# Kernel optimization log

Measured on AMD Instinct MI355X. Metric: run time of the kernel, lower is better.

The kernel has to match this reference:

```python
import jax, jax.numpy as jnp
import numpy as np

B, N, K, D = 256, 64, 12, 128


def setup_inputs() -> dict:
    key = jax.random.key(0)
    ks = jax.random.split(key, 12)
    s = 1.0 / np.sqrt(D)
    inp = {
        "nodes_hidden": jax.random.normal(ks[0], (B, N, D), jnp.float32),
        "neighbors_hidden": jax.random.normal(ks[1], (B, N, K, D), jnp.float32),
        # binary neighbor-validity mask (float, as in the torch code)
        "mask": (jax.random.uniform(ks[2], (B, N, K)) < 0.7).astype(jnp.float32),
        "Wq": jax.random.uniform(ks[3], (D, D), jnp.float32, -s, s),
        "bq": jax.random.uniform(ks[4], (D,), jnp.float32, -s, s),
        "Wk": jax.random.uniform(ks[5], (D, D), jnp.float32, -s, s),
        "bk": jax.random.uniform(ks[6], (D,), jnp.float32, -s, s),
        "Wv": jax.random.uniform(ks[7], (D, D), jnp.float32, -s, s),
        "bv": jax.random.uniform(ks[8], (D,), jnp.float32, -s, s),
        # W_att: Linear(2D -> 1); split into the query half and key half of its weight
        "wa_q": jax.random.uniform(ks[9], (D,), jnp.float32, -s, s),
        "wa_k": jax.random.uniform(ks[10], (D,), jnp.float32, -s, s),
        "ba": jax.random.uniform(ks[11], (), jnp.float32, -s, s),
    }
    return inp


def reference(nodes_hidden, neighbors_hidden, mask, Wq, bq, Wk, bk, Wv, bv, wa_q, wa_k, ba):
    # prepend the node itself to its neighbor list: [B,N,K+1,D]
    nh = jnp.concatenate([nodes_hidden[:, :, None, :], neighbors_hidden], axis=2)
    # prepend an always-valid slot to the mask: [B,N,K+1]
    m = jnp.concatenate([jnp.ones(mask.shape[:-1] + (1,), mask.dtype), mask], axis=-1)

    q = nodes_hidden @ Wq + bq            # [B,N,D]
    k = nh @ Wk + bk                      # [B,N,K+1,D]
    v = nh @ Wv + bv                      # [B,N,K+1,D]

    # W_att(cat([q,k])) == q.wa_q + k.wa_k + ba  (avoids materializing the 2D concat)
    sim = (q @ wa_q)[:, :, None] + k @ wa_k + ba   # [B,N,K+1]
    sim = jnp.where(sim >= 0, sim, 0.2 * sim)      # LeakyReLU(0.2)
    sim = jnp.exp(sim) * m                         # masked exp (matches torch exactly)
    attn = sim / (jnp.sum(sim, axis=-1, keepdims=True) + 1e-16)
    return jnp.einsum('bnk,bnkd->bnd', attn, v)    # [B,N,D]
```

## Files before the change

### kernel.cpp

```cpp
#include <hip/hip_runtime.h>


#define B_  256
#define N_  64
#define K_  12
#define D_  128
#define BN  (B_ * N_)
#define ROWS 8
#define HB_STRIDE 132

__global__ void prep_kernel(const float* __restrict__ Wq, const float* __restrict__ bq,
                            const float* __restrict__ Wk, const float* __restrict__ bk,
                            const float* __restrict__ wa_q, const float* __restrict__ wa_k,
                            float* __restrict__ ws) {
    int g = blockIdx.x;
    int l = threadIdx.x;
    const float* row;
    const float* wa;
    float* outp;
    if (g < 128)      { row = Wq + g * D_;         wa = wa_q; outp = ws + g; }
    else if (g < 256) { row = Wk + (g - 128) * D_; wa = wa_k; outp = ws + 128 + (g - 128); }
    else if (g == 256){ row = bq;                  wa = wa_q; outp = ws + 256; }
    else              { row = bk;                  wa = wa_k; outp = ws + 257; }

    float2 r = ((const float2*)row)[l];
    float2 w = ((const float2*)wa)[l];
    float p = r.x * w.x + r.y * w.y;
    #pragma unroll
    for (int m = 1; m < 64; m <<= 1) p += __shfl_xor(p, m, 64);
    if (l == 0) *outp = p;
}

__global__ void __launch_bounds__(256, 4)
fused_kernel(const float* __restrict__ nodes, const float* __restrict__ neigh,
             const float* __restrict__ mask, const float* __restrict__ ba_p,
             const float* __restrict__ ws, const float* __restrict__ Wv,
             const float* __restrict__ bv, float* __restrict__ out) {
    __shared__ float hb[ROWS * HB_STRIDE];
    __shared__ float scL[ROWS];

    const int t    = threadIdx.x;
    const int wave = t >> 6;
    const int l    = t & 63;
    const int li   = l & 31;
    const int h    = l >> 5;
    const int j8   = l & 7;

    const float cq  = ws[256];
    const float ckb = ws[257];
    const float ba  = ba_p[0];
    const float cst = cq + ckb + ba;
    const float4 wqe4 = ((const float4*)ws)[li];
    const float4 wke4 = ((const float4*)(ws + 128))[li];

    for (int p = 0; p < 2; ++p) {
        const int lrow = wave * 2 + p;
        const int idx  = blockIdx.x * ROWS + lrow;

        const float4 nv = ((const float4*)(nodes + (size_t)idx * D_))[li];
        const float4* gp4 = (const float4*)(neigh + (size_t)idx * (K_ * D_));
        float4 x[6];
        #pragma unroll
        for (int i = 0; i < 6; ++i) x[i] = gp4[i * 64 + l];
        const float mval = (j8 < 6) ? mask[(size_t)idx * K_ + 2 * j8 + h] : 0.0f;

        float v[8];
        v[7] = nv.x*wqe4.x + nv.y*wqe4.y + nv.z*wqe4.z + nv.w*wqe4.w;
        v[6] = nv.x*wke4.x + nv.y*wke4.y + nv.z*wke4.z + nv.w*wke4.w;
        #pragma unroll
        for (int i = 0; i < 6; ++i)
            v[i] = x[i].x*wke4.x + x[i].y*wke4.y + x[i].z*wke4.z + x[i].w*wke4.w;

        float a0, a1, a2, a3;
        {
            const bool hi = (l & 1);
            float g0 = hi ? v[0] : v[1];
            float g1 = hi ? v[2] : v[3];
            float g2 = hi ? v[4] : v[5];
            float g3 = hi ? v[6] : v[7];
            g0 = __shfl_xor(g0, 1, 64);
            g1 = __shfl_xor(g1, 1, 64);
            g2 = __shfl_xor(g2, 1, 64);
            g3 = __shfl_xor(g3, 1, 64);
            a0 = (hi ? v[1] : v[0]) + g0;
            a1 = (hi ? v[3] : v[2]) + g1;
            a2 = (hi ? v[5] : v[4]) + g2;
            a3 = (hi ? v[7] : v[6]) + g3;
        }
        float b0, b1;
        {
            const bool hi = (l & 2);
            float g0 = hi ? a0 : a1;
            float g1 = hi ? a2 : a3;
            g0 = __shfl_xor(g0, 2, 64);
            g1 = __shfl_xor(g1, 2, 64);
            b0 = (hi ? a1 : a0) + g0;
            b1 = (hi ? a3 : a2) + g1;
        }
        float c;
        {
            const bool hi = (l & 4);
            float g = hi ? b0 : b1;
            g = __shfl_xor(g, 4, 64);
            c = (hi ? b1 : b0) + g;
        }
        c += __shfl_xor(c, 8, 64);
        c += __shfl_xor(c, 16, 64);

        const float pq  = __shfl(c, 7, 8);
        const float pkn = __shfl(c, 6, 8);
        const float base = pq + cst;

        float s0 = base + pkn;
        s0 = (s0 >= 0.0f) ? s0 : 0.2f * s0;
        const float e0 = __expf(s0);

        float sj = base + c;
        sj = (sj >= 0.0f) ? sj : 0.2f * sj;
        const float ej = (j8 < 6) ? __expf(sj) * mval : 0.0f;

        float Sn = ej;
        Sn += __shfl_xor(Sn, 1, 64);
        Sn += __shfl_xor(Sn, 2, 64);
        Sn += __shfl_xor(Sn, 4, 64);
        Sn += __shfl_xor(Sn, 32, 64);
        const float S   = e0 + Sn;
        const float inv = 1.0f / (S + 1e-16f);
        const float aj  = ej * inv;

        const float an = (h == 0) ? e0 * inv : 0.0f;
        float4 acc;
        acc.x = an * nv.x; acc.y = an * nv.y; acc.z = an * nv.z; acc.w = an * nv.w;
        #pragma unroll
        for (int i = 0; i < 6; ++i) {
            const float ai = __shfl(aj, i, 8);
            acc.x += ai * x[i].x;
            acc.y += ai * x[i].y;
            acc.z += ai * x[i].z;
            acc.w += ai * x[i].w;
        }
        acc.x += __shfl_xor(acc.x, 32, 64);
        acc.y += __shfl_xor(acc.y, 32, 64);
        acc.z += __shfl_xor(acc.z, 32, 64);
        acc.w += __shfl_xor(acc.w, 32, 64);

        if (h == 0) {
            *(float4*)(hb + lrow * HB_STRIDE + 4 * li) = acc;
            if (li == 0) scL[lrow] = S * inv;
        }
    }
    __syncthreads();

    const int rg = t >> 5;
    const int cg = t & 31;
    const float4* wv4 = (const float4*)Wv;
    const float* hrow = hb + rg * HB_STRIDE;

    float4 vacc = make_float4(0.0f, 0.0f, 0.0f, 0.0f);
    #pragma unroll 8
    for (int k = 0; k < D_; ++k) {
        const float a  = hrow[k];
        const float4 w = wv4[k * 32 + cg];
        vacc.x += a * w.x;
        vacc.y += a * w.y;
        vacc.z += a * w.z;
        vacc.w += a * w.w;
    }

    const float4 bvv = ((const float4*)bv)[cg];
    const float  s   = scL[rg];
    float4 o;
    o.x = vacc.x + bvv.x * s;
    o.y = vacc.y + bvv.y * s;
    o.z = vacc.z + bvv.z * s;
    o.w = vacc.w + bvv.w * s;
    *(float4*)(out + (size_t)(blockIdx.x * ROWS + rg) * D_ + cg * 4) = o;
}

extern "C" void kernel_launch(void* const* d_in, const int* in_sizes, int n_in,
                              void* d_out, int out_size, void* d_ws, size_t ws_size,
                              hipStream_t stream) {
    const float* nodes = (const float*)d_in[0];
    const float* neigh = (const float*)d_in[1];
    const float* mask  = (const float*)d_in[2];
    const float* Wq    = (const float*)d_in[3];
    const float* bq    = (const float*)d_in[4];
    const float* Wk    = (const float*)d_in[5];
    const float* bk    = (const float*)d_in[6];
    const float* Wv    = (const float*)d_in[7];
    const float* bv    = (const float*)d_in[8];
    const float* wa_q  = (const float*)d_in[9];
    const float* wa_k  = (const float*)d_in[10];
    const float* ba    = (const float*)d_in[11];
    float* out = (float*)d_out;
    float* ws  = (float*)d_ws;

    prep_kernel<<<258, 64, 0, stream>>>(Wq, bq, Wk, bk, wa_q, wa_k, ws);
    fused_kernel<<<BN / ROWS, 256, 0, stream>>>(nodes, neigh, mask, ba, ws, Wv, bv, out);
}
```

Before: 201.0 us.

## Interleave two rows per wave and defer softmax normalization

Each wave now issues the global loads for both of its rows up front and interleaves their reductions and shuffles, so memory latency for the second row overlaps the first. The softmax sum is taken from the same shuffled weights used to accumulate the weighted values, and normalization is applied once at the end, removing a serial shuffle-reduction before accumulation. The occupancy hint in launch bounds is dropped and the Wv matmul loop unroll is raised. Holding twice the loaded data in registers increases register pressure and may reduce occupancy.

```diff
diff --git a/kernel.cpp b/kernel.cpp
--- a/kernel.cpp
+++ b/kernel.cpp
@@ -31,7 +31,7 @@
     if (l == 0) *outp = p;
 }
 
-__global__ void __launch_bounds__(256, 4)
+__global__ void __launch_bounds__(256)
 fused_kernel(const float* __restrict__ nodes, const float* __restrict__ neigh,
              const float* __restrict__ mask, const float* __restrict__ ba_p,
              const float* __restrict__ ws, const float* __restrict__ Wv,
@@ -53,99 +53,141 @@
     const float4 wqe4 = ((const float4*)ws)[li];
     const float4 wke4 = ((const float4*)(ws + 128))[li];
 
-    for (int p = 0; p < 2; ++p) {
-        const int lrow = wave * 2 + p;
-        const int idx  = blockIdx.x * ROWS + lrow;
-
-        const float4 nv = ((const float4*)(nodes + (size_t)idx * D_))[li];
+    const int idx0 = blockIdx.x * ROWS + wave * 2;
+
+    float4 nv[2];
+    float4 x[2][6];
+    float  mv[2];
+    #pragma unroll
+    for (int p = 0; p < 2; ++p) {
+        const int idx = idx0 + p;
+        nv[p] = ((const float4*)(nodes + (size_t)idx * D_))[li];
         const float4* gp4 = (const float4*)(neigh + (size_t)idx * (K_ * D_));
-        float4 x[6];
-        #pragma unroll
-        for (int i = 0; i < 6; ++i) x[i] = gp4[i * 64 + l];
-        const float mval = (j8 < 6) ? mask[(size_t)idx * K_ + 2 * j8 + h] : 0.0f;
-
-        float v[8];
-        v[7] = nv.x*wqe4.x + nv.y*wqe4.y + nv.z*wqe4.z + nv.w*wqe4.w;
-        v[6] = nv.x*wke4.x + nv.y*wke4.y + nv.z*wke4.z + nv.w*wke4.w;
+        #pragma unroll
+        for (int i = 0; i < 6; ++i) x[p][i] = gp4[i * 64 + l];
+        mv[p] = (j8 < 6) ? mask[(size_t)idx * K_ + 2 * j8 + h] : 0.0f;
+    }
+
+    float v[2][8];
+    #pragma unroll
+    for (int p = 0; p < 2; ++p) {
+        v[p][7] = nv[p].x*wqe4.x + nv[p].y*wqe4.y + nv[p].z*wqe4.z + nv[p].w*wqe4.w;
+        v[p][6] = nv[p].x*wke4.x + nv[p].y*wke4.y + nv[p].z*wke4.z + nv[p].w*wke4.w;
         #pragma unroll
         for (int i = 0; i < 6; ++i)
-            v[i] = x[i].x*wke4.x + x[i].y*wke4.y + x[i].z*wke4.z + x[i].w*wke4.w;
-
-        float a0, a1, a2, a3;
-        {
-            const bool hi = (l & 1);
-            float g0 = hi ? v[0] : v[1];
-            float g1 = hi ? v[2] : v[3];
-            float g2 = hi ? v[4] : v[5];
-            float g3 = hi ? v[6] : v[7];
+            v[p][i] = x[p][i].x*wke4.x + x[p][i].y*wke4.y
+                    + x[p][i].z*wke4.z + x[p][i].w*wke4.w;
+    }
+
+    float A[2][4];
+    {
+        const bool hi = (l & 1);
+        #pragma unroll
+        for (int p = 0; p < 2; ++p) {
+            float g0 = hi ? v[p][0] : v[p][1];
+            float g1 = hi ? v[p][2] : v[p][3];
+            float g2 = hi ? v[p][4] : v[p][5];
+            float g3 = hi ? v[p][6] : v[p][7];
             g0 = __shfl_xor(g0, 1, 64);
             g1 = __shfl_xor(g1, 1, 64);
             g2 = __shfl_xor(g2, 1, 64);
             g3 = __shfl_xor(g3, 1, 64);
-            a0 = (hi ? v[1] : v[0]) + g0;
-            a1 = (hi ? v[3] : v[2]) + g1;
-            a2 = (hi ? v[5] : v[4]) + g2;
-            a3 = (hi ? v[7] : v[6]) + g3;
-        }
-        float b0, b1;
-        {
-            const bool hi = (l & 2);
-            float g0 = hi ? a0 : a1;
-            float g1 = hi ? a2 : a3;
+            A[p][0] = (hi ? v[p][1] : v[p][0]) + g0;
+            A[p][1] = (hi ? v[p][3] : v[p][2]) + g1;
+            A[p][2] = (hi ? v[p][5] : v[p][4]) + g2;
+            A[p][3] = (hi ? v[p][7] : v[p][6]) + g3;
+        }
+    }
+    float Bs[2][2];
+    {
+        const bool hi = (l & 2);
+        #pragma unroll
+        for (int p = 0; p < 2; ++p) {
+            float g0 = hi ? A[p][0] : A[p][1];
+            float g1 = hi ? A[p][2] : A[p][3];
             g0 = __shfl_xor(g0, 2, 64);
             g1 = __shfl_xor(g1, 2, 64);
-            b0 = (hi ? a1 : a0) + g0;
-            b1 = (hi ? a3 : a2) + g1;
-        }
-        float c;
-        {
-            const bool hi = (l & 4);
-            float g = hi ? b0 : b1;
+            Bs[p][0] = (hi ? A[p][1] : A[p][0]) + g0;
+            Bs[p][1] = (hi ? A[p][3] : A[p][2]) + g1;
+        }
+    }
+    float c[2];
+    {
+        const bool hi = (l & 4);
+        #pragma unroll
+        for (int p = 0; p < 2; ++p) {
+            float g = hi ? Bs[p][0] : Bs[p][1];
             g = __shfl_xor(g, 4, 64);
-            c = (hi ? b1 : b0) + g;
-        }
-        c += __shfl_xor(c, 8, 64);
-        c += __shfl_xor(c, 16, 64);
-
-        const float pq  = __shfl(c, 7, 8);
-        const float pkn = __shfl(c, 6, 8);
-        const float base = pq + cst;
-
-        float s0 = base + pkn;
+            c[p] = (hi ? Bs[p][1] : Bs[p][0]) + g;
+        }
+    }
+    #pragma unroll
+    for (int p = 0; p < 2; ++p) c[p] += __shfl_xor(c[p], 8, 64);
+    #pragma unroll
+    for (int p = 0; p < 2; ++p) c[p] += __shfl_xor(c[p], 16, 64);
+
+    float pq[2], pkn[2];
+    #pragma unroll
+    for (int p = 0; p < 2; ++p) {
+        pq[p]  = __shfl(c[p], 7, 8);
+        pkn[p] = __shfl(c[p], 6, 8);
+    }
+
+    float e0[2], ej[2];
+    #pragma unroll
+    for (int p = 0; p < 2; ++p) {
+        const float base = pq[p] + cst;
+        float s0 = base + pkn[p];
         s0 = (s0 >= 0.0f) ? s0 : 0.2f * s0;
-        const float e0 = __expf(s0);
-
-        float sj = base + c;
+        e0[p] = __expf(s0);
+        float sj = base + c[p];
         sj = (sj >= 0.0f) ? sj : 0.2f * sj;
-        const float ej = (j8 < 6) ? __expf(sj) * mval : 0.0f;
-
-        float Sn = ej;
-        Sn += __shfl_xor(Sn, 1, 64);
-        Sn += __shfl_xor(Sn, 2, 64);
-        Sn += __shfl_xor(Sn, 4, 64);
-        Sn += __shfl_xor(Sn, 32, 64);
-        const float S   = e0 + Sn;
+        ej[p] = (j8 < 6) ? __expf(sj) * mv[p] : 0.0f;
+    }
+
+    float4 acc[2];
+    float  Se[2];
+    #pragma unroll
+    for (int p = 0; p < 2; ++p) {
+        const float an = (h == 0) ? e0[p] : 0.0f;
+        acc[p].x = an * nv[p].x;
+        acc[p].y = an * nv[p].y;
+        acc[p].z = an * nv[p].z;
+        acc[p].w = an * nv[p].w;
+        Se[p] = 0.0f;
+    }
+    #pragma unroll
+    for (int i = 0; i < 6; ++i) {
+        #pragma unroll
+        for (int p = 0; p < 2; ++p) {
+            const float bi = __shfl(ej[p], i, 8);
+            acc[p].x += bi * x[p][i].x;
+            acc[p].y += bi * x[p][i].y;
+            acc[p].z += bi * x[p][i].z;
+            acc[p].w += bi * x[p][i].w;
+            Se[p]    += bi;
+        }
+    }
+    #pragma unroll
+    for (int p = 0; p < 2; ++p) {
+        acc[p].x += __shfl_xor(acc[p].x, 32, 64);
+        acc[p].y += __shfl_xor(acc[p].y, 32, 64);
+        acc[p].z += __shfl_xor(acc[p].z, 32, 64);
+        acc[p].w += __shfl_xor(acc[p].w, 32, 64);
+        Se[p]    += __shfl_xor(Se[p],    32, 64);
+    }
+    #pragma unroll
+    for (int p = 0; p < 2; ++p) {
+        const float S   = e0[p] + Se[p];
         const float inv = 1.0f / (S + 1e-16f);
-        const float aj  = ej * inv;
-
-        const float an = (h == 0) ? e0 * inv : 0.0f;
-        float4 acc;
-        acc.x = an * nv.x; acc.y = an * nv.y; acc.z = an * nv.z; acc.w = an * nv.w;
-        #pragma unroll
-        for (int i = 0; i < 6; ++i) {
-            const float ai = __shfl(aj, i, 8);
-            acc.x += ai * x[i].x;
-            acc.y += ai * x[i].y;
-            acc.z += ai * x[i].z;
-            acc.w += ai * x[i].w;
-        }
-        acc.x += __shfl_xor(acc.x, 32, 64);
-        acc.y += __shfl_xor(acc.y, 32, 64);
-        acc.z += __shfl_xor(acc.z, 32, 64);
-        acc.w += __shfl_xor(acc.w, 32, 64);
-
         if (h == 0) {
-            *(float4*)(hb + lrow * HB_STRIDE + 4 * li) = acc;
+            const int lrow = wave * 2 + p;
+            float4 o;
+            o.x = acc[p].x * inv;
+            o.y = acc[p].y * inv;
+            o.z = acc[p].z * inv;
+            o.w = acc[p].w * inv;
+            *(float4*)(hb + lrow * HB_STRIDE + 4 * li) = o;
             if (li == 0) scL[lrow] = S * inv;
         }
     }
@@ -157,7 +199,7 @@
     const float* hrow = hb + rg * HB_STRIDE;
 
     float4 vacc = make_float4(0.0f, 0.0f, 0.0f, 0.0f);
-    #pragma unroll 8
+    #pragma unroll 16
     for (int k = 0; k < D_; ++k) {
         const float a  = hrow[k];
         const float4 w = wv4[k * 32 + cg];
```

New measurement: 199.1 us. Within noise of the previous version (-0.9%).

## Double-buffer neighbor loads, process 16 rows per block, reuse Wv across rows

Applied to the files above, without the earlier changes.

Each wave now handles four rows instead of two. The next row's neighbor and node data is prefetched into a second register buffer while the current row is computed, and scheduling barriers and asm pins keep the compiler from merging the two phases. Softmax normalisation is deferred: unnormalised weights are accumulated and the result is scaled once at the end. The Wv projection now computes two rows per thread, so each Wv load is reused twice and LDS reads are vectorised. The cost is higher register pressure, which may lower occupancy under the launch bounds, and half as many blocks.

```diff
diff --git a/kernel.cpp b/kernel.cpp
--- a/kernel.cpp
+++ b/kernel.cpp
@@ -6,8 +6,11 @@
 #define K_  12
 #define D_  128
 #define BN  (B_ * N_)
-#define ROWS 8
+#define ROWS 16
 #define HB_STRIDE 132
+
+#define PIN4(v)  asm volatile("" : "+v"(v.x), "+v"(v.y), "+v"(v.z), "+v"(v.w))
+#define PIN1(s)  asm volatile("" : "+v"(s))
 
 __global__ void prep_kernel(const float* __restrict__ Wq, const float* __restrict__ bq,
                             const float* __restrict__ Wk, const float* __restrict__ bk,
@@ -53,25 +56,47 @@
     const float4 wqe4 = ((const float4*)ws)[li];
     const float4 wke4 = ((const float4*)(ws + 128))[li];
 
-    for (int p = 0; p < 2; ++p) {
-        const int lrow = wave * 2 + p;
-        const int idx  = blockIdx.x * ROWS + lrow;
-
-        const float4 nv = ((const float4*)(nodes + (size_t)idx * D_))[li];
-        const float4* gp4 = (const float4*)(neigh + (size_t)idx * (K_ * D_));
-        float4 x[6];
+    const int idx0 = blockIdx.x * ROWS + wave * 4;
+
+    float4 xb[2][6];
+    float4 nv[2];
+    float  mv[2];
+
+    #define LOADP(buf, pi) do {                                              \
+        const int idx_ = idx0 + (pi);                                        \
+        nv[buf] = ((const float4*)(nodes + (size_t)idx_ * D_))[li];          \
+        const float4* gp_ = (const float4*)(neigh + (size_t)idx_ * (K_*D_)); \
+        xb[buf][0] = gp_[0 * 64 + l];                                        \
+        xb[buf][1] = gp_[1 * 64 + l];                                        \
+        xb[buf][2] = gp_[2 * 64 + l];                                        \
+        xb[buf][3] = gp_[3 * 64 + l];                                        \
+        xb[buf][4] = gp_[4 * 64 + l];                                        \
+        xb[buf][5] = gp_[5 * 64 + l];                                        \
+        mv[buf] = (j8 < 6) ? mask[(size_t)idx_ * K_ + 2 * j8 + h] : 0.0f;    \
+    } while (0)
+
+    LOADP(0, 0);
+
+    #pragma unroll
+    for (int i = 0; i < 4; ++i) {
+        const int b  = i & 1;
+        const int nb = b ^ 1;
+        if (i < 3) LOADP(nb, i + 1);
+        __builtin_amdgcn_sched_barrier(0);
+
+        float v[8];
+        v[7] = nv[b].x*wqe4.x + nv[b].y*wqe4.y + nv[b].z*wqe4.z + nv[b].w*wqe4.w;
+        v[6] = nv[b].x*wke4.x + nv[b].y*wke4.y + nv[b].z*wke4.z + nv[b].w*wke4.w;
         #pragma unroll
-        for (int i = 0; i < 6; ++i) x[i] = gp4[i * 64 + l];
-        const float mval = (j8 < 6) ? mask[(size_t)idx * K_ + 2 * j8 + h] : 0.0f;
-
-        float v[8];
-        v[7] = nv.x*wqe4.x + nv.y*wqe4.y + nv.z*wqe4.z + nv.w*wqe4.w;
-        v[6] = nv.x*wke4.x + nv.y*wke4.y + nv.z*wke4.z + nv.w*wke4.w;
-        #pragma unroll
-        for (int i = 0; i < 6; ++i)
-            v[i] = x[i].x*wke4.x + x[i].y*wke4.y + x[i].z*wke4.z + x[i].w*wke4.w;
-
-        float a0, a1, a2, a3;
+        for (int q = 0; q < 6; ++q)
+            v[q] = xb[b][q].x*wke4.x + xb[b][q].y*wke4.y
+                 + xb[b][q].z*wke4.z + xb[b][q].w*wke4.w;
+
+        PIN4(xb[b][0]); PIN4(xb[b][1]); PIN4(xb[b][2]);
+        PIN4(xb[b][3]); PIN4(xb[b][4]); PIN4(xb[b][5]);
+        PIN4(nv[b]);    PIN1(mv[b]);
+
+        float A0, A1, A2, A3;
         {
             const bool hi = (l & 1);
             float g0 = hi ? v[0] : v[1];
@@ -82,27 +107,27 @@
             g1 = __shfl_xor(g1, 1, 64);
             g2 = __shfl_xor(g2, 1, 64);
             g3 = __shfl_xor(g3, 1, 64);
-            a0 = (hi ? v[1] : v[0]) + g0;
-            a1 = (hi ? v[3] : v[2]) + g1;
-            a2 = (hi ? v[5] : v[4]) + g2;
-            a3 = (hi ? v[7] : v[6]) + g3;
-        }
-        float b0, b1;
+            A0 = (hi ? v[1] : v[0]) + g0;
+            A1 = (hi ? v[3] : v[2]) + g1;
+            A2 = (hi ? v[5] : v[4]) + g2;
+            A3 = (hi ? v[7] : v[6]) + g3;
+        }
+        float B0, B1;
         {
             const bool hi = (l & 2);
-            float g0 = hi ? a0 : a1;
-            float g1 = hi ? a2 : a3;
+            float g0 = hi ? A0 : A1;
+            float g1 = hi ? A2 : A3;
             g0 = __shfl_xor(g0, 2, 64);
             g1 = __shfl_xor(g1, 2, 64);
-            b0 = (hi ? a1 : a0) + g0;
-            b1 = (hi ? a3 : a2) + g1;
+            B0 = (hi ? A1 : A0) + g0;
+            B1 = (hi ? A3 : A2) + g1;
         }
         float c;
         {
             const bool hi = (l & 4);
-            float g = hi ? b0 : b1;
+            float g = hi ? B0 : B1;
             g = __shfl_xor(g, 4, 64);
-            c = (hi ? b1 : b0) + g;
+            c = (hi ? B1 : B0) + g;
         }
         c += __shfl_xor(c, 8, 64);
         c += __shfl_xor(c, 16, 64);
@@ -114,67 +139,92 @@
         float s0 = base + pkn;
         s0 = (s0 >= 0.0f) ? s0 : 0.2f * s0;
         const float e0 = __expf(s0);
-
         float sj = base + c;
         sj = (sj >= 0.0f) ? sj : 0.2f * sj;
-        const float ej = (j8 < 6) ? __expf(sj) * mval : 0.0f;
-
-        float Sn = ej;
-        Sn += __shfl_xor(Sn, 1, 64);
-        Sn += __shfl_xor(Sn, 2, 64);
-        Sn += __shfl_xor(Sn, 4, 64);
-        Sn += __shfl_xor(Sn, 32, 64);
-        const float S   = e0 + Sn;
-        const float inv = 1.0f / (S + 1e-16f);
-        const float aj  = ej * inv;
-
-        const float an = (h == 0) ? e0 * inv : 0.0f;
+        const float ej = (j8 < 6) ? __expf(sj) * mv[b] : 0.0f;
+
+        const float an = (h == 0) ? e0 : 0.0f;
         float4 acc;
-        acc.x = an * nv.x; acc.y = an * nv.y; acc.z = an * nv.z; acc.w = an * nv.w;
+        acc.x = an * nv[b].x;
+        acc.y = an * nv[b].y;
+        acc.z = an * nv[b].z;
+        acc.w = an * nv[b].w;
+        float Se = 0.0f;
         #pragma unroll
-        for (int i = 0; i < 6; ++i) {
-            const float ai = __shfl(aj, i, 8);
-            acc.x += ai * x[i].x;
-            acc.y += ai * x[i].y;
-            acc.z += ai * x[i].z;
-            acc.w += ai * x[i].w;
+        for (int q = 0; q < 6; ++q) {
+            const float bi = __shfl(ej, q, 8);
+            acc.x += bi * xb[b][q].x;
+            acc.y += bi * xb[b][q].y;
+            acc.z += bi * xb[b][q].z;
+            acc.w += bi * xb[b][q].w;
+            Se    += bi;
         }
         acc.x += __shfl_xor(acc.x, 32, 64);
         acc.y += __shfl_xor(acc.y, 32, 64);
         acc.z += __shfl_xor(acc.z, 32, 64);
         acc.w += __shfl_xor(acc.w, 32, 64);
-
+        Se    += __shfl_xor(Se,    32, 64);
+
+        const float S   = e0 + Se;
+        const float inv = 1.0f / (S + 1e-16f);
         if (h == 0) {
-            *(float4*)(hb + lrow * HB_STRIDE + 4 * li) = acc;
+            const int lrow = wave * 4 + i;
+            float4 o;
+            o.x = acc.x * inv;
+            o.y = acc.y * inv;
+            o.z = acc.z * inv;
+            o.w = acc.w * inv;
+            *(float4*)(hb + lrow * HB_STRIDE + 4 * li) = o;
             if (li == 0) scL[lrow] = S * inv;
         }
     }
+    #undef LOADP
     __syncthreads();
 
     const int rg = t >> 5;
     const int cg = t & 31;
     const float4* wv4 = (const float4*)Wv;
-    const float* hrow = hb + rg * HB_STRIDE;
-
-    float4 vacc = make_float4(0.0f, 0.0f, 0.0f, 0.0f);
+    const float* hr0 = hb + rg * HB_STRIDE;
+    const float* hr1 = hb + (rg + 8) * HB_STRIDE;
+
+    float4 acc0 = make_float4(0.0f, 0.0f, 0.0f, 0.0f);
+    float4 acc1 = make_float4(0.0f, 0.0f, 0.0f, 0.0f);
     #pragma unroll 8
-    for (int k = 0; k < D_; ++k) {
-        const float a  = hrow[k];
-        const float4 w = wv4[k * 32 + cg];
-        vacc.x += a * w.x;
-        vacc.y += a * w.y;
-        vacc.z += a * w.z;
-        vacc.w += a * w.w;
+    for (int kq = 0; kq < 32; ++kq) {
+        const float4 a0 = *(const float4*)(hr0 + 4 * kq);
+        const float4 a1 = *(const float4*)(hr1 + 4 * kq);
+        #pragma unroll
+        for (int e = 0; e < 4; ++e) {
+            const float4 w = wv4[(4 * kq + e) * 32 + cg];
+            const float f0 = (e == 0) ? a0.x : (e == 1) ? a0.y : (e == 2) ? a0.z : a0.w;
+            const float f1 = (e == 0) ? a1.x : (e == 1) ? a1.y : (e == 2) ? a1.z : a1.w;
+            acc0.x += f0 * w.x; acc0.y += f0 * w.y;
+            acc0.z += f0 * w.z; acc0.w += f0 * w.w;
+            acc1.x += f1 * w.x; acc1.y += f1 * w.y;
+            acc1.z += f1 * w.z; acc1.w += f1 * w.w;
+        }
     }
 
     const float4 bvv = ((const float4*)bv)[cg];
-    const float  s   = scL[rg];
-    float4 o;
-    o.x = vacc.x + bvv.x * s;
-    o.y = vacc.y + bvv.y * s;
-    o.z = vacc.z + bvv.z * s;
-    o.w = vacc.w + bvv.w * s;
-    *(float4*)(out + (size_t)(blockIdx.x * ROWS + rg) * D_ + cg * 4) = o;
+    const int row0 = blockIdx.x * ROWS;
+    {
+        const float s = scL[rg];
+        float4 o;
+        o.x = acc0.x + bvv.x * s;
+        o.y = acc0.y + bvv.y * s;
+        o.z = acc0.z + bvv.z * s;
+        o.w = acc0.w + bvv.w * s;
+        *(float4*)(out + (size_t)(row0 + rg) * D_ + cg * 4) = o;
+    }
+    {
+        const float s = scL[rg + 8];
+        float4 o;
+        o.x = acc1.x + bvv.x * s;
+        o.y = acc1.y + bvv.y * s;
+        o.z = acc1.z + bvv.z * s;
+        o.w = acc1.w + bvv.w * s;
+        *(float4*)(out + (size_t)(row0 + rg + 8) * D_ + cg * 4) = o;
+    }
 }
 
 extern "C" void kernel_launch(void* const* d_in, const int* in_sizes, int n_in,
```

Measured after the change: 188.8 us. -6.1%, faster.

## Map each half-wave to one row and issue all neighbor loads at once

Applied to the files above, without the earlier changes.

Rather than looping twice per wave with 64 lanes per row, each 32-lane half-wave now handles one row and loads all 12 neighbor vectors up front. The point is to put more loads in flight and drop the per-row loop. The score reduction grows to a 16-way transpose-style shuffle tree, and normalization moves to a single multiply at the end. The Wv GEMV now reads the hidden row from LDS as float4, and inline-asm pins plus a waves_per_eu attribute steer register allocation. The cost is higher register pressure per thread.

```diff
diff --git a/kernel.cpp b/kernel.cpp
--- a/kernel.cpp
+++ b/kernel.cpp
@@ -8,6 +8,8 @@
 #define BN  (B_ * N_)
 #define ROWS 8
 #define HB_STRIDE 132
+
+#define PIN4(v)  asm volatile("" : "+v"(v.x), "+v"(v.y), "+v"(v.z), "+v"(v.w))
 
 __global__ void prep_kernel(const float* __restrict__ Wq, const float* __restrict__ bq,
                             const float* __restrict__ Wk, const float* __restrict__ bk,
@@ -31,7 +33,8 @@
     if (l == 0) *outp = p;
 }
 
-__global__ void __launch_bounds__(256, 4)
+__global__ void __launch_bounds__(256)
+__attribute__((amdgpu_waves_per_eu(4, 4)))
 fused_kernel(const float* __restrict__ nodes, const float* __restrict__ neigh,
              const float* __restrict__ mask, const float* __restrict__ ba_p,
              const float* __restrict__ ws, const float* __restrict__ Wv,
@@ -43,8 +46,9 @@
     const int wave = t >> 6;
     const int l    = t & 63;
     const int li   = l & 31;
-    const int h    = l >> 5;
-    const int j8   = l & 7;
+    const int hf   = l >> 5;
+    const int g    = li & 15;
+    const int hsel = l & 32;
 
     const float cq  = ws[256];
     const float ckb = ws[257];
@@ -53,102 +57,105 @@
     const float4 wqe4 = ((const float4*)ws)[li];
     const float4 wke4 = ((const float4*)(ws + 128))[li];
 
-    for (int p = 0; p < 2; ++p) {
-        const int lrow = wave * 2 + p;
-        const int idx  = blockIdx.x * ROWS + lrow;
-
-        const float4 nv = ((const float4*)(nodes + (size_t)idx * D_))[li];
-        const float4* gp4 = (const float4*)(neigh + (size_t)idx * (K_ * D_));
-        float4 x[6];
-        #pragma unroll
-        for (int i = 0; i < 6; ++i) x[i] = gp4[i * 64 + l];
-        const float mval = (j8 < 6) ? mask[(size_t)idx * K_ + 2 * j8 + h] : 0.0f;
-
-        float v[8];
-        v[7] = nv.x*wqe4.x + nv.y*wqe4.y + nv.z*wqe4.z + nv.w*wqe4.w;
-        v[6] = nv.x*wke4.x + nv.y*wke4.y + nv.z*wke4.z + nv.w*wke4.w;
-        #pragma unroll
-        for (int i = 0; i < 6; ++i)
-            v[i] = x[i].x*wke4.x + x[i].y*wke4.y + x[i].z*wke4.z + x[i].w*wke4.w;
-
-        float a0, a1, a2, a3;
-        {
-            const bool hi = (l & 1);
-            float g0 = hi ? v[0] : v[1];
-            float g1 = hi ? v[2] : v[3];
-            float g2 = hi ? v[4] : v[5];
-            float g3 = hi ? v[6] : v[7];
-            g0 = __shfl_xor(g0, 1, 64);
-            g1 = __shfl_xor(g1, 1, 64);
-            g2 = __shfl_xor(g2, 1, 64);
-            g3 = __shfl_xor(g3, 1, 64);
-            a0 = (hi ? v[1] : v[0]) + g0;
-            a1 = (hi ? v[3] : v[2]) + g1;
-            a2 = (hi ? v[5] : v[4]) + g2;
-            a3 = (hi ? v[7] : v[6]) + g3;
-        }
-        float b0, b1;
-        {
-            const bool hi = (l & 2);
-            float g0 = hi ? a0 : a1;
-            float g1 = hi ? a2 : a3;
-            g0 = __shfl_xor(g0, 2, 64);
-            g1 = __shfl_xor(g1, 2, 64);
-            b0 = (hi ? a1 : a0) + g0;
-            b1 = (hi ? a3 : a2) + g1;
-        }
-        float c;
-        {
-            const bool hi = (l & 4);
-            float g = hi ? b0 : b1;
-            g = __shfl_xor(g, 4, 64);
-            c = (hi ? b1 : b0) + g;
-        }
-        c += __shfl_xor(c, 8, 64);
-        c += __shfl_xor(c, 16, 64);
-
-        const float pq  = __shfl(c, 7, 8);
-        const float pkn = __shfl(c, 6, 8);
-        const float base = pq + cst;
-
-        float s0 = base + pkn;
-        s0 = (s0 >= 0.0f) ? s0 : 0.2f * s0;
-        const float e0 = __expf(s0);
-
-        float sj = base + c;
-        sj = (sj >= 0.0f) ? sj : 0.2f * sj;
-        const float ej = (j8 < 6) ? __expf(sj) * mval : 0.0f;
-
-        float Sn = ej;
-        Sn += __shfl_xor(Sn, 1, 64);
-        Sn += __shfl_xor(Sn, 2, 64);
-        Sn += __shfl_xor(Sn, 4, 64);
-        Sn += __shfl_xor(Sn, 32, 64);
-        const float S   = e0 + Sn;
-        const float inv = 1.0f / (S + 1e-16f);
-        const float aj  = ej * inv;
-
-        const float an = (h == 0) ? e0 * inv : 0.0f;
-        float4 acc;
-        acc.x = an * nv.x; acc.y = an * nv.y; acc.z = an * nv.z; acc.w = an * nv.w;
-        #pragma unroll
-        for (int i = 0; i < 6; ++i) {
-            const float ai = __shfl(aj, i, 8);
-            acc.x += ai * x[i].x;
-            acc.y += ai * x[i].y;
-            acc.z += ai * x[i].z;
-            acc.w += ai * x[i].w;
-        }
-        acc.x += __shfl_xor(acc.x, 32, 64);
-        acc.y += __shfl_xor(acc.y, 32, 64);
-        acc.z += __shfl_xor(acc.z, 32, 64);
-        acc.w += __shfl_xor(acc.w, 32, 64);
-
-        if (h == 0) {
-            *(float4*)(hb + lrow * HB_STRIDE + 4 * li) = acc;
-            if (li == 0) scL[lrow] = S * inv;
-        }
-    }
+    const int idx = blockIdx.x * ROWS + wave * 2 + hf;
+
+    const float4* gp = (const float4*)(neigh + (size_t)idx * (K_ * D_));
+    float4 xv[K_];
+    #pragma unroll
+    for (int j = 0; j < K_; ++j) xv[j] = gp[j * 32 + li];
+    const float4 nv = ((const float4*)(nodes + (size_t)idx * D_))[li];
+    const float mval = (g < K_) ? mask[(size_t)idx * K_ + g]
+                                : ((g == 12) ? 1.0f : 0.0f);
+
+    float v[16];
+    #pragma unroll
+    for (int j = 0; j < K_; ++j)
+        v[j] = xv[j].x*wke4.x + xv[j].y*wke4.y + xv[j].z*wke4.z + xv[j].w*wke4.w;
+    v[12] = nv.x*wke4.x + nv.y*wke4.y + nv.z*wke4.z + nv.w*wke4.w;
+    v[13] = nv.x*wqe4.x + nv.y*wqe4.y + nv.z*wqe4.z + nv.w*wqe4.w;
+    v[14] = 0.0f;
+    v[15] = 0.0f;
+
+    PIN4(xv[0]); PIN4(xv[1]); PIN4(xv[2]);  PIN4(xv[3]);
+    PIN4(xv[4]); PIN4(xv[5]); PIN4(xv[6]);  PIN4(xv[7]);
+    PIN4(xv[8]); PIN4(xv[9]); PIN4(xv[10]); PIN4(xv[11]);
+
+    float r8[8];
+    {
+        const bool hi = (l & 1);
+        #pragma unroll
+        for (int m = 0; m < 8; ++m) {
+            float take = hi ? v[2*m] : v[2*m + 1];
+            float keep = hi ? v[2*m + 1] : v[2*m];
+            r8[m] = keep + __shfl_xor(take, 1, 64);
+        }
+    }
+    float r4[4];
+    {
+        const bool hi = (l & 2);
+        #pragma unroll
+        for (int m = 0; m < 4; ++m) {
+            float take = hi ? r8[2*m] : r8[2*m + 1];
+            float keep = hi ? r8[2*m + 1] : r8[2*m];
+            r4[m] = keep + __shfl_xor(take, 2, 64);
+        }
+    }
+    float r2[2];
+    {
+        const bool hi = (l & 4);
+        #pragma unroll
+        for (int m = 0; m < 2; ++m) {
+            float take = hi ? r4[2*m] : r4[2*m + 1];
+            float keep = hi ? r4[2*m + 1] : r4[2*m];
+            r2[m] = keep + __shfl_xor(take, 4, 64);
+        }
+    }
+    float c;
+    {
+        const bool hi = (l & 8);
+        float take = hi ? r2[0] : r2[1];
+        float keep = hi ? r2[1] : r2[0];
+        c = keep + __shfl_xor(take, 8, 64);
+    }
+    c += __shfl_xor(c, 16, 64);
+
+    const float pq  = __shfl(c, hsel | 13, 64);
+    const float pkn = __shfl(c, hsel | 12, 64);
+    (void)pkn;
+    const float base = pq + cst;
+    float s_own = base + c;
+    s_own = (s_own >= 0.0f) ? s_own : 0.2f * s_own;
+    const float e_own = __expf(s_own) * mval;
+
+    float S;
+    float4 acc;
+    {
+        const float en = __shfl(e_own, hsel | 12, 64);
+        acc.x = en * nv.x;
+        acc.y = en * nv.y;
+        acc.z = en * nv.z;
+        acc.w = en * nv.w;
+        S = en;
+    }
+    #pragma unroll
+    for (int j = 0; j < K_; ++j) {
+        const float ej = __shfl(e_own, hsel | j, 64);
+        acc.x += ej * xv[j].x;
+        acc.y += ej * xv[j].y;
+        acc.z += ej * xv[j].z;
+        acc.w += ej * xv[j].w;
+        S += ej;
+    }
+    const float inv = 1.0f / (S + 1e-16f);
+
+    const int lrow = wave * 2 + hf;
+    float4 o;
+    o.x = acc.x * inv;
+    o.y = acc.y * inv;
+    o.z = acc.z * inv;
+    o.w = acc.w * inv;
+    *(float4*)(hb + lrow * HB_STRIDE + 4 * li) = o;
+    if (li == 0) scL[lrow] = S * inv;
     __syncthreads();
 
     const int rg = t >> 5;
@@ -158,23 +165,27 @@
 
     float4 vacc = make_float4(0.0f, 0.0f, 0.0f, 0.0f);
     #pragma unroll 8
-    for (int k = 0; k < D_; ++k) {
-        const float a  = hrow[k];
-        const float4 w = wv4[k * 32 + cg];
-        vacc.x += a * w.x;
-        vacc.y += a * w.y;
-        vacc.z += a * w.z;
-        vacc.w += a * w.w;
+    for (int kq = 0; kq < 32; ++kq) {
+        const float4 a = *(const float4*)(hrow + 4 * kq);
+        #pragma unroll
+        for (int e = 0; e < 4; ++e) {
+            const float4 w = wv4[(4 * kq + e) * 32 + cg];
+            const float f = (e == 0) ? a.x : (e == 1) ? a.y : (e == 2) ? a.z : a.w;
+            vacc.x += f * w.x;
+            vacc.y += f * w.y;
+            vacc.z += f * w.z;
+            vacc.w += f * w.w;
+        }
     }
 
     const float4 bvv = ((const float4*)bv)[cg];
     const float  s   = scL[rg];
-    float4 o;
-    o.x = vacc.x + bvv.x * s;
-    o.y = vacc.y + bvv.y * s;
-    o.z = vacc.z + bvv.z * s;
-    o.w = vacc.w + bvv.w * s;
-    *(float4*)(out + (size_t)(blockIdx.x * ROWS + rg) * D_ + cg * 4) = o;
+    float4 o2;
+    o2.x = vacc.x + bvv.x * s;
+    o2.y = vacc.y + bvv.y * s;
+    o2.z = vacc.z + bvv.z * s;
+    o2.w = vacc.w + bvv.w * s;
+    *(float4*)(out + (size_t)(blockIdx.x * ROWS + rg) * D_ + cg * 4) = o2;
 }
 
 extern "C" void kernel_launch(void* const* d_in, const int* in_sizes, int n_in,
```

New measurement: 208.6 us. 3.8% more time.
